# Optimization experiments

Hardware: AMD Instinct MI355X
Metric: run time of the kernel (lower is better)

The kernel has to match this reference:

```python
import jax, jax.numpy as jnp
import numpy as np

B, A, RF, F = 4096, 128, 128, 128  # batch, max_atom, res_n_features, n_features


def setup_inputs() -> dict:
    key = jax.random.key(0)
    k1, k2, k3, k4 = jax.random.split(key, 4)
    node_features = jax.random.normal(k1, (B, A, F), dtype=jnp.float32)
    residual_features = jax.random.normal(k2, (B, A, RF), dtype=jnp.float32)
    # Glorot-style init for the residual transform weight
    scale = jnp.sqrt(6.0 / (RF + F)).astype(jnp.float32)
    w = jax.random.uniform(k3, (RF, F), dtype=jnp.float32, minval=-scale, maxval=scale)
    # mol_slice[g] = [n_atoms_g, n_features]; atom counts vary per graph (ragged)
    atoms = jax.random.randint(k4, (B,), 1, A + 1, dtype=jnp.int64)
    mol_slice = jnp.stack([atoms, jnp.full((B,), F, dtype=jnp.int64)], axis=1)
    return {"node_features": node_features, "residual_features": residual_features,
            "w": w, "mol_slice": mol_slice}


def reference(node_features, residual_features, w, mol_slice):
    # Original: per-graph slice to [M_g, F], x_res @ w + x, pad back to max_atom,
    # then relu. Equivalent masked batched form: rows >= M_g become zeros.
    M = mol_slice[:, 0]  # [B] atom counts
    row_mask = (jnp.arange(A)[None, :] < M[:, None])[:, :, None]  # [B, A, 1]
    y = jnp.einsum('bar,rf->baf', residual_features, w) + node_features  # [B, A, F]
    return jnp.where(row_mask, jax.nn.relu(y), jnp.zeros((), dtype=y.dtype))
```

## Files before the change

kernel.cpp:

```cpp
#include <hip/hip_runtime.h>


typedef __bf16 bf16x8 __attribute__((ext_vector_type(8)));
typedef float f32x4 __attribute__((ext_vector_type(4)));

static_assert(sizeof(bf16x8) == 16, "bf16x8 must be 16B");
static_assert(sizeof(f32x4) == 16, "f32x4 must be 16B");

__global__ __launch_bounds__(256) void wT_kernel(const float* __restrict__ w,
                                                 __bf16* __restrict__ wT) {
    int i = blockIdx.x * 256 + threadIdx.x;
    int f = i >> 7;
    int r = i & 127;
    wT[i] = (__bf16)w[r * 128 + f];
}

__global__ __launch_bounds__(256) void blockend_kernel(
    const float* __restrict__ node,
    const float* __restrict__ resid,
    const __bf16* __restrict__ wT,
    const int*   __restrict__ mol,
    float*       __restrict__ out)
{
    const int b    = blockIdx.x;
    const int t    = threadIdx.x;
    const int wave = t >> 6;
    const int lane = t & 63;
    const int quad = lane >> 4;
    const int m16  = lane & 15;

    const int M      = mol[2 * b];
    const int a_base = wave * 32;

    const size_t base = (size_t)b * (128 * 128);
    float* outW = out + base + (size_t)a_base * 128;

    if (M <= a_base) {
        f32x4 z = {0.f, 0.f, 0.f, 0.f};
        f32x4* p = (f32x4*)outW;
#pragma unroll
        for (int it = 0; it < 16; ++it)
            p[it * 64 + lane] = z;
        return;
    }

    const float* residW = resid + base + (size_t)a_base * 128;
    const float* nodeW  = node  + base + (size_t)a_base * 128;

    f32x4 acc[2][8];
#pragma unroll
    for (int nt = 0; nt < 2; ++nt)
#pragma unroll
        for (int ft = 0; ft < 8; ++ft)
            acc[nt][ft] = (f32x4){0.f, 0.f, 0.f, 0.f};

#pragma unroll
    for (int kk = 0; kk < 4; ++kk) {
        const int k0 = kk * 32 + quad * 8;

        bf16x8 rfrag[2];
#pragma unroll
        for (int nt = 0; nt < 2; ++nt) {
            const float* ap = residW + (nt * 16 + m16) * 128 + k0;
            f32x4 lo = *(const f32x4*)ap;
            f32x4 hi = *(const f32x4*)(ap + 4);
            bf16x8 v;
            v[0] = (__bf16)lo[0]; v[1] = (__bf16)lo[1];
            v[2] = (__bf16)lo[2]; v[3] = (__bf16)lo[3];
            v[4] = (__bf16)hi[0]; v[5] = (__bf16)hi[1];
            v[6] = (__bf16)hi[2]; v[7] = (__bf16)hi[3];
            rfrag[nt] = v;
        }

#pragma unroll
        for (int ft = 0; ft < 8; ++ft) {
            bf16x8 wfrag = *(const bf16x8*)(wT + (ft * 16 + m16) * 128 + k0);
#pragma unroll
            for (int nt = 0; nt < 2; ++nt)
                acc[nt][ft] = __builtin_amdgcn_mfma_f32_16x16x32_bf16(
                    wfrag, rfrag[nt], acc[nt][ft], 0, 0, 0);
        }
    }

#pragma unroll
    for (int nt = 0; nt < 2; ++nt) {
        const int a_local = nt * 16 + m16;
        const bool active = (a_base + a_local) < M;
#pragma unroll
        for (int ft = 0; ft < 8; ++ft) {
            const int off = a_local * 128 + ft * 16 + quad * 4;
            f32x4 v = {0.f, 0.f, 0.f, 0.f};
            if (active) {
                f32x4 nd = *(const f32x4*)(nodeW + off);
#pragma unroll
                for (int i = 0; i < 4; ++i) {
                    float x = acc[nt][ft][i] + nd[i];
                    v[i] = x > 0.f ? x : 0.f;
                }
            }
            *(f32x4*)(outW + off) = v;
        }
    }
}

extern "C" void kernel_launch(void* const* d_in, const int* in_sizes, int n_in,
                              void* d_out, int out_size, void* d_ws, size_t ws_size,
                              hipStream_t stream) {
    const float* node  = (const float*)d_in[0];
    const float* resid = (const float*)d_in[1];
    const float* w     = (const float*)d_in[2];
    const int*   mol   = (const int*)d_in[3];
    float*       out   = (float*)d_out;
    __bf16*      wT    = (__bf16*)d_ws;

    wT_kernel<<<64, 256, 0, stream>>>(w, wT);
    blockend_kernel<<<4096, 256, 0, stream>>>(node, resid, wT, mol, out);
}
```

Baseline: 572.8 us.

## Split each graph across two blocks with 16-row waves and nontemporal stores

Measured after the change: 650.1 us. 1.13x slower.

```diff
diff --git a/kernel.cpp b/kernel.cpp
--- a/kernel.cpp
+++ b/kernel.cpp
@@ -15,14 +15,15 @@
     wT[i] = (__bf16)w[r * 128 + f];
 }
 
-__global__ __launch_bounds__(256) void blockend_kernel(
+__global__ __launch_bounds__(256, 4) void blockend_kernel(
     const float* __restrict__ node,
     const float* __restrict__ resid,
     const __bf16* __restrict__ wT,
     const int*   __restrict__ mol,
     float*       __restrict__ out)
 {
-    const int b    = blockIdx.x;
+    const int bb   = blockIdx.x;
+    const int b    = bb >> 1;
     const int t    = threadIdx.x;
     const int wave = t >> 6;
     const int lane = t & 63;
@@ -30,76 +31,56 @@
     const int m16  = lane & 15;
 
     const int M      = mol[2 * b];
-    const int a_base = wave * 32;
+    const int a_base = (bb & 1) * 64 + wave * 16;
 
     const size_t base = (size_t)b * (128 * 128);
     float* outW = out + base + (size_t)a_base * 128;
 
     if (M <= a_base) {
         f32x4 z = {0.f, 0.f, 0.f, 0.f};
-        f32x4* p = (f32x4*)outW;
 #pragma unroll
-        for (int it = 0; it < 16; ++it)
-            p[it * 64 + lane] = z;
+        for (int it = 0; it < 8; ++it)
+            __builtin_nontemporal_store(z, (f32x4*)outW + it * 64 + lane);
         return;
     }
+
+    const bool active = (a_base + m16) < M;
+    const int  rrow   = active ? m16 : 0;
 
     const float* residW = resid + base + (size_t)a_base * 128;
     const float* nodeW  = node  + base + (size_t)a_base * 128;
 
-    f32x4 acc[2][8];
-#pragma unroll
-    for (int nt = 0; nt < 2; ++nt)
-#pragma unroll
-        for (int ft = 0; ft < 8; ++ft)
-            acc[nt][ft] = (f32x4){0.f, 0.f, 0.f, 0.f};
-
+    bf16x8 rfrag[4];
 #pragma unroll
     for (int kk = 0; kk < 4; ++kk) {
-        const int k0 = kk * 32 + quad * 8;
-
-        bf16x8 rfrag[2];
-#pragma unroll
-        for (int nt = 0; nt < 2; ++nt) {
-            const float* ap = residW + (nt * 16 + m16) * 128 + k0;
-            f32x4 lo = *(const f32x4*)ap;
-            f32x4 hi = *(const f32x4*)(ap + 4);
-            bf16x8 v;
-            v[0] = (__bf16)lo[0]; v[1] = (__bf16)lo[1];
-            v[2] = (__bf16)lo[2]; v[3] = (__bf16)lo[3];
-            v[4] = (__bf16)hi[0]; v[5] = (__bf16)hi[1];
-            v[6] = (__bf16)hi[2]; v[7] = (__bf16)hi[3];
-            rfrag[nt] = v;
-        }
-
-#pragma unroll
-        for (int ft = 0; ft < 8; ++ft) {
-            bf16x8 wfrag = *(const bf16x8*)(wT + (ft * 16 + m16) * 128 + k0);
-#pragma unroll
-            for (int nt = 0; nt < 2; ++nt)
-                acc[nt][ft] = __builtin_amdgcn_mfma_f32_16x16x32_bf16(
-                    wfrag, rfrag[nt], acc[nt][ft], 0, 0, 0);
-        }
+        const float* ap = residW + rrow * 128 + kk * 32 + quad * 8;
+        f32x4 lo = *(const f32x4*)ap;
+        f32x4 hi = *(const f32x4*)(ap + 4);
+        bf16x8 v;
+        v[0] = (__bf16)lo[0]; v[1] = (__bf16)lo[1];
+        v[2] = (__bf16)lo[2]; v[3] = (__bf16)lo[3];
+        v[4] = (__bf16)hi[0]; v[5] = (__bf16)hi[1];
+        v[6] = (__bf16)hi[2]; v[7] = (__bf16)hi[3];
+        rfrag[kk] = v;
     }
 
 #pragma unroll
-    for (int nt = 0; nt < 2; ++nt) {
-        const int a_local = nt * 16 + m16;
-        const bool active = (a_base + a_local) < M;
+    for (int ft = 0; ft < 8; ++ft) {
+        f32x4 acc = {0.f, 0.f, 0.f, 0.f};
 #pragma unroll
-        for (int ft = 0; ft < 8; ++ft) {
-            const int off = a_local * 128 + ft * 16 + quad * 4;
-            f32x4 v = {0.f, 0.f, 0.f, 0.f};
-            if (active) {
-                f32x4 nd = *(const f32x4*)(nodeW + off);
+        for (int kk = 0; kk < 4; ++kk) {
+            bf16x8 wfrag = *(const bf16x8*)(wT + (ft * 16 + m16) * 128 + kk * 32 + quad * 8);
+            acc = __builtin_amdgcn_mfma_f32_16x16x32_bf16(wfrag, rfrag[kk], acc, 0, 0, 0);
+        }
+        const int offs = ft * 16 + quad * 4;
+        f32x4 nd = *(const f32x4*)(nodeW + rrow * 128 + offs);
+        f32x4 v;
 #pragma unroll
-                for (int i = 0; i < 4; ++i) {
-                    float x = acc[nt][ft][i] + nd[i];
-                    v[i] = x > 0.f ? x : 0.f;
-                }
-            }
-            *(f32x4*)(outW + off) = v;
+        for (int i = 0; i < 4; ++i) {
+            float x = acc[i] + nd[i];
+            v[i] = (active && x > 0.f) ? x : 0.f;
         }
+        __builtin_nontemporal_store(v, (f32x4*)(outW + m16 * 128 + offs));
     }
 }
 
@@ -114,5 +95,5 @@
     __bf16*      wT    = (__bf16*)d_ws;
 
     wT_kernel<<<64, 256, 0, stream>>>(w, wT);
-    blockend_kernel<<<4096, 256, 0, stream>>>(node, resid, wT, mol, out);
+    blockend_kernel<<<8192, 256, 0, stream>>>(node, resid, wT, mol, out);
 }
```

## Stage swizzled bf16 weight in LDS and hoist residual/node loads before barrier

Applied to the files above, without the earlier changes.

Result: faster. 551.2 us (-3.8%).

```diff
diff --git a/kernel.cpp b/kernel.cpp
--- a/kernel.cpp
+++ b/kernel.cpp
@@ -8,20 +8,25 @@
 static_assert(sizeof(f32x4) == 16, "f32x4 must be 16B");
 
 __global__ __launch_bounds__(256) void wT_kernel(const float* __restrict__ w,
-                                                 __bf16* __restrict__ wT) {
-    int i = blockIdx.x * 256 + threadIdx.x;
-    int f = i >> 7;
-    int r = i & 127;
-    wT[i] = (__bf16)w[r * 128 + f];
+                                                 __bf16* __restrict__ wTs) {
+    int i  = blockIdx.x * 256 + threadIdx.x;
+    int f  = i >> 7;
+    int k  = i & 127;
+    int cu = k >> 3;
+    int j  = k & 7;
+    int r  = ((cu ^ (f & 7)) << 3) | j;
+    wTs[i] = (__bf16)w[r * 128 + f];
 }
 
-__global__ __launch_bounds__(256) void blockend_kernel(
+__global__ __launch_bounds__(256, 3) void blockend_kernel(
     const float* __restrict__ node,
     const float* __restrict__ resid,
-    const __bf16* __restrict__ wT,
+    const __bf16* __restrict__ wTs,
     const int*   __restrict__ mol,
     float*       __restrict__ out)
 {
+    __shared__ __align__(16) unsigned char lds[32768];
+
     const int b    = blockIdx.x;
     const int t    = threadIdx.x;
     const int wave = t >> 6;
@@ -29,13 +34,57 @@
     const int quad = lane >> 4;
     const int m16  = lane & 15;
 
-    const int M      = mol[2 * b];
-    const int a_base = wave * 32;
+    const int M       = mol[2 * b];
+    const int a_base  = wave * 32;
+    const size_t base = (size_t)b * (128 * 128);
 
-    const size_t base = (size_t)b * (128 * 128);
+#pragma unroll
+    for (int i = 0; i < 8; ++i) {
+        bf16x8 v = *(const bf16x8*)(wTs + (i * 256 + t) * 8);
+        *(bf16x8*)(lds + i * 4096 + t * 16) = v;
+    }
+
+    const bool worker = (M > a_base);
+
+    bool act0 = false, act1 = false;
+    int  rr0 = 0, rr1 = 0;
+    f32x4 rl[2][4], rh[2][4];
+    f32x4 nd0[8];
+
+    if (worker) {
+        act0 = (a_base + m16) < M;
+        act1 = (a_base + 16 + m16) < M;
+        rr0  = act0 ? m16        : 0;
+        rr1  = act1 ? (16 + m16) : 0;
+
+        const float* rowR0 = resid + base + (size_t)(a_base + rr0) * 128;
+        const float* rowR1 = resid + base + (size_t)(a_base + rr1) * 128;
+#pragma unroll
+        for (int kk = 0; kk < 4; ++kk) {
+            rl[0][kk] = *(const f32x4*)(rowR0 + kk * 32 + quad * 8);
+            rh[0][kk] = *(const f32x4*)(rowR0 + kk * 32 + quad * 8 + 4);
+            rl[1][kk] = *(const f32x4*)(rowR1 + kk * 32 + quad * 8);
+            rh[1][kk] = *(const f32x4*)(rowR1 + kk * 32 + quad * 8 + 4);
+        }
+        const float* rowN0 = node + base + (size_t)(a_base + rr0) * 128;
+#pragma unroll
+        for (int ft = 0; ft < 8; ++ft)
+            nd0[ft] = *(const f32x4*)(rowN0 + ft * 16 + quad * 4);
+
+#pragma unroll
+        for (int kk = 0; kk < 4; ++kk)
+            asm volatile("" : "+v"(rl[0][kk]), "+v"(rh[0][kk]),
+                              "+v"(rl[1][kk]), "+v"(rh[1][kk]));
+#pragma unroll
+        for (int ft = 0; ft < 8; ++ft)
+            asm volatile("" : "+v"(nd0[ft]));
+    }
+
+    __syncthreads();
+
     float* outW = out + base + (size_t)a_base * 128;
 
-    if (M <= a_base) {
+    if (!worker) {
         f32x4 z = {0.f, 0.f, 0.f, 0.f};
         f32x4* p = (f32x4*)outW;
 #pragma unroll
@@ -44,8 +93,24 @@
         return;
     }
 
-    const float* residW = resid + base + (size_t)a_base * 128;
-    const float* nodeW  = node  + base + (size_t)a_base * 128;
+    bf16x8 rfrag[2][4];
+#pragma unroll
+    for (int nt = 0; nt < 2; ++nt)
+#pragma unroll
+        for (int kk = 0; kk < 4; ++kk) {
+            bf16x8 v;
+            v[0] = (__bf16)rl[nt][kk][0]; v[1] = (__bf16)rl[nt][kk][1];
+            v[2] = (__bf16)rl[nt][kk][2]; v[3] = (__bf16)rl[nt][kk][3];
+            v[4] = (__bf16)rh[nt][kk][0]; v[5] = (__bf16)rh[nt][kk][1];
+            v[6] = (__bf16)rh[nt][kk][2]; v[7] = (__bf16)rh[nt][kk][3];
+            rfrag[nt][kk] = v;
+        }
+
+    const int xr = m16 & 7;
+    int raddr[4];
+#pragma unroll
+    for (int kk = 0; kk < 4; ++kk)
+        raddr[kk] = m16 * 256 + ((((kk << 2) | quad) ^ xr) << 4);
 
     f32x4 acc[2][8];
 #pragma unroll
@@ -55,51 +120,47 @@
             acc[nt][ft] = (f32x4){0.f, 0.f, 0.f, 0.f};
 
 #pragma unroll
-    for (int kk = 0; kk < 4; ++kk) {
-        const int k0 = kk * 32 + quad * 8;
-
-        bf16x8 rfrag[2];
+    for (int ft = 0; ft < 8; ++ft) {
 #pragma unroll
-        for (int nt = 0; nt < 2; ++nt) {
-            const float* ap = residW + (nt * 16 + m16) * 128 + k0;
-            f32x4 lo = *(const f32x4*)ap;
-            f32x4 hi = *(const f32x4*)(ap + 4);
-            bf16x8 v;
-            v[0] = (__bf16)lo[0]; v[1] = (__bf16)lo[1];
-            v[2] = (__bf16)lo[2]; v[3] = (__bf16)lo[3];
-            v[4] = (__bf16)hi[0]; v[5] = (__bf16)hi[1];
-            v[6] = (__bf16)hi[2]; v[7] = (__bf16)hi[3];
-            rfrag[nt] = v;
-        }
-
-#pragma unroll
-        for (int ft = 0; ft < 8; ++ft) {
-            bf16x8 wfrag = *(const bf16x8*)(wT + (ft * 16 + m16) * 128 + k0);
-#pragma unroll
-            for (int nt = 0; nt < 2; ++nt)
-                acc[nt][ft] = __builtin_amdgcn_mfma_f32_16x16x32_bf16(
-                    wfrag, rfrag[nt], acc[nt][ft], 0, 0, 0);
+        for (int kk = 0; kk < 4; ++kk) {
+            bf16x8 wfrag = *(const bf16x8*)(lds + ft * 4096 + raddr[kk]);
+            acc[0][ft] = __builtin_amdgcn_mfma_f32_16x16x32_bf16(
+                wfrag, rfrag[0][kk], acc[0][ft], 0, 0, 0);
+            acc[1][ft] = __builtin_amdgcn_mfma_f32_16x16x32_bf16(
+                wfrag, rfrag[1][kk], acc[1][ft], 0, 0, 0);
         }
     }
 
+    f32x4 nd1[8];
+    const float* rowN1 = node + base + (size_t)(a_base + rr1) * 128;
 #pragma unroll
-    for (int nt = 0; nt < 2; ++nt) {
-        const int a_local = nt * 16 + m16;
-        const bool active = (a_base + a_local) < M;
+    for (int ft = 0; ft < 8; ++ft)
+        nd1[ft] = *(const f32x4*)(rowN1 + ft * 16 + quad * 4);
 #pragma unroll
-        for (int ft = 0; ft < 8; ++ft) {
-            const int off = a_local * 128 + ft * 16 + quad * 4;
-            f32x4 v = {0.f, 0.f, 0.f, 0.f};
-            if (active) {
-                f32x4 nd = *(const f32x4*)(nodeW + off);
+    for (int ft = 0; ft < 8; ++ft)
+        asm volatile("" : "+v"(nd1[ft]));
+
 #pragma unroll
-                for (int i = 0; i < 4; ++i) {
-                    float x = acc[nt][ft][i] + nd[i];
-                    v[i] = x > 0.f ? x : 0.f;
-                }
-            }
-            *(f32x4*)(outW + off) = v;
+    for (int ft = 0; ft < 8; ++ft) {
+        const int off = m16 * 128 + ft * 16 + quad * 4;
+        f32x4 v;
+#pragma unroll
+        for (int i = 0; i < 4; ++i) {
+            float x = acc[0][ft][i] + nd0[ft][i];
+            v[i] = (act0 && x > 0.f) ? x : 0.f;
         }
+        *(f32x4*)(outW + off) = v;
+    }
+#pragma unroll
+    for (int ft = 0; ft < 8; ++ft) {
+        const int off = (16 + m16) * 128 + ft * 16 + quad * 4;
+        f32x4 v;
+#pragma unroll
+        for (int i = 0; i < 4; ++i) {
+            float x = acc[1][ft][i] + nd1[ft][i];
+            v[i] = (act1 && x > 0.f) ? x : 0.f;
+        }
+        *(f32x4*)(outW + off) = v;
     }
 }
 
@@ -111,8 +172,8 @@
     const float* w     = (const float*)d_in[2];
     const int*   mol   = (const int*)d_in[3];
     float*       out   = (float*)d_out;
-    __bf16*      wT    = (__bf16*)d_ws;
+    __bf16*      wTs   = (__bf16*)d_ws;
 
-    wT_kernel<<<64, 256, 0, stream>>>(w, wT);
-    blockend_kernel<<<4096, 256, 0, stream>>>(node, resid, wT, mol, out);
+    wT_kernel<<<64, 256, 0, stream>>>(w, wTs);
+    blockend_kernel<<<4096, 256, 0, stream>>>(node, resid, wTs, mol, out);
 }
```
